# Kernel optimization log

Measured on AMD Instinct MI355X. Metric: run time of the kernel, lower is better.

Reference implementation:

```python
import jax, jax.numpy as jnp
import numpy as np

N_NODES = 100000
N_EDGES = 200000
N_GRAPHS = 4096
NODE_DIM = 256
OUT_DIM = 768
LAYERS = 4
NODE_FEATS = 9
EDGE_FEATS = 3
NODE_VOCAB = 119  # max categorical size across node features (padded)
EDGE_VOCAB = 22   # max categorical size across edge features (padded)


def setup_inputs() -> dict:
    key = jax.random.key(0)
    ks = jax.random.split(key, 16)
    x_cat = jax.random.randint(ks[0], (N_NODES, NODE_FEATS), 0, 2)
    edge_attr = jax.random.randint(ks[1], (N_EDGES, EDGE_FEATS), 0, 2)
    edge_index = jax.random.randint(ks[2], (2, N_EDGES), 0, N_NODES)
    batch = jnp.sort(jax.random.randint(ks[3], (N_NODES,), 0, N_GRAPHS))
    s = 0.02
    node_emb = jax.random.normal(ks[4], (NODE_FEATS, NODE_VOCAB, NODE_DIM), jnp.float32) * s
    edge_emb = jax.random.normal(ks[5], (EDGE_FEATS, EDGE_VOCAB, NODE_DIM), jnp.float32) * s
    W1 = jax.random.normal(ks[6], (LAYERS, NODE_DIM, 2 * NODE_DIM), jnp.float32) * s
    b1 = jnp.zeros((LAYERS, 2 * NODE_DIM), jnp.float32)
    W2 = jax.random.normal(ks[7], (LAYERS, 2 * NODE_DIM, NODE_DIM), jnp.float32) * s
    b2 = jnp.zeros((LAYERS, NODE_DIM), jnp.float32)
    pW1 = jax.random.normal(ks[8], (NODE_DIM, NODE_DIM), jnp.float32) * s
    pb1 = jnp.zeros((NODE_DIM,), jnp.float32)
    pW2 = jax.random.normal(ks[9], (NODE_DIM, OUT_DIM), jnp.float32) * s
    pb2 = jnp.zeros((OUT_DIM,), jnp.float32)
    return {
        "x_cat": x_cat, "edge_attr": edge_attr, "edge_index": edge_index, "batch": batch,
        "node_emb": node_emb, "edge_emb": edge_emb,
        "W1": W1, "b1": b1, "W2": W2, "b2": b2,
        "pW1": pW1, "pb1": pb1, "pW2": pW2, "pb2": pb2,
    }


def _encode(tables, idx):
    # tables: [F, V, D], idx: [N, F] -> sum over features of embedding lookups -> [N, D]
    return jnp.sum(jax.vmap(lambda tbl, i: tbl[i], in_axes=(0, 1))(tables, idx), axis=0)


def reference(x_cat, edge_attr, edge_index, batch, node_emb, edge_emb,
              W1, b1, W2, b2, pW1, pb1, pW2, pb2):
    x = _encode(node_emb, x_cat)          # [N, D]
    e = _encode(edge_emb, edge_attr)      # [E, D]
    src, dst = edge_index[0], edge_index[1]
    for l in range(LAYERS):
        # GINEConv: aggr = sum_{j in N(i)} relu(x_j + e_ij); out = mlp((1+eps)*x_i + aggr), eps=0
        msg = jax.nn.relu(x[src] + e)                                  # [E, D]
        agg = jax.ops.segment_sum(msg, dst, num_segments=N_NODES)     # [N, D]
        h = x + agg
        h = jax.nn.relu(h @ W1[l] + b1[l]) @ W2[l] + b2[l]
        x = jax.nn.relu(h)
    g = jax.ops.segment_sum(x, batch, num_segments=N_GRAPHS)          # [G, D]
    g = jax.nn.relu(g @ pW1 + pb1) @ pW2 + pb2                         # [G, OUT]
    norm = jnp.maximum(jnp.linalg.norm(g, axis=-1, keepdims=True), 1e-12)
    return g / norm
```

## Files before the change

kernel.cpp:

```cpp
#include <hip/hip_runtime.h>

#define N_NODES 100000
#define N_NODES_PAD 100032
#define N_EDGES 200000
#define N_GRAPHS 4096
#define D 256
#define D2 512
#define OUTD 768
#define LAYERS 4
#define NODE_FEATS 9
#define EDGE_FEATS 3
#define NODE_VOCAB 119
#define EDGE_VOCAB 22
#define BM 64
#define GB 8

typedef __attribute__((ext_vector_type(8))) short bf16x8;
typedef __attribute__((ext_vector_type(4))) float f32x4;
typedef unsigned short ushort_t;
typedef unsigned int uint_t;

__device__ __forceinline__ ushort_t f2b(float f) {
    union { float f; uint_t u; } x; x.f = f;
    uint_t r = (x.u + 0x7FFFu + ((x.u >> 16) & 1u)) >> 16;
    return (ushort_t)r;
}
__device__ __forceinline__ float b2f(ushort_t u) {
    union { uint_t u; float f; } x; x.u = ((uint_t)u) << 16;
    return x.f;
}

__device__ __forceinline__ int lower_bound_i(const int* a, int n, int v) {
    int lo = 0, hi = n;
    while (lo < hi) { int mid = (lo + hi) >> 1; if (a[mid] < v) lo = mid + 1; else hi = mid; }
    return lo;
}

__global__ __launch_bounds__(256) void encode_nodes_k(const int* __restrict__ xcat,
                                                      const float* __restrict__ tab,
                                                      ushort_t* __restrict__ X) {
    int n = blockIdx.x, d = threadIdx.x;
    float acc = 0.f;
#pragma unroll
    for (int f = 0; f < NODE_FEATS; ++f) {
        int idx = xcat[n * NODE_FEATS + f];
        acc += tab[((size_t)f * NODE_VOCAB + idx) * D + d];
    }
    X[(size_t)n * D + d] = f2b(acc);
}

__global__ __launch_bounds__(256) void count_k(const int* __restrict__ eidx, int* deg) {
    int e = blockIdx.x * 256 + threadIdx.x;
    if (e < N_EDGES) atomicAdd(&deg[eidx[N_EDGES + e]], 1);
}

#define SCAN_B 1024
__global__ __launch_bounds__(256) void scan1_k(const int* __restrict__ deg,
                                               int* __restrict__ excl, int* __restrict__ bsum) {
    __shared__ int sh[256];
    int b = blockIdx.x, t = threadIdx.x;
    int base = b * SCAN_B + t * 4;
    int d0 = (base + 0) < N_NODES ? deg[base + 0] : 0;
    int d1 = (base + 1) < N_NODES ? deg[base + 1] : 0;
    int d2 = (base + 2) < N_NODES ? deg[base + 2] : 0;
    int d3 = (base + 3) < N_NODES ? deg[base + 3] : 0;
    int s = d0 + d1 + d2 + d3;
    sh[t] = s; __syncthreads();
    for (int off = 1; off < 256; off <<= 1) {
        int x = (t >= off) ? sh[t - off] : 0;
        __syncthreads();
        sh[t] += x;
        __syncthreads();
    }
    int incl = sh[t];
    int ex = incl - s;
    if (base + 0 < N_NODES) excl[base + 0] = ex;
    if (base + 1 < N_NODES) excl[base + 1] = ex + d0;
    if (base + 2 < N_NODES) excl[base + 2] = ex + d0 + d1;
    if (base + 3 < N_NODES) excl[base + 3] = ex + d0 + d1 + d2;
    if (t == 255) bsum[b] = incl;
}

__global__ void scan2_k(int* bsum, int nb) {
    __shared__ int sh[128];
    int t = threadIdx.x;
    int v = (t < nb) ? bsum[t] : 0;
    sh[t] = v; __syncthreads();
    for (int off = 1; off < 128; off <<= 1) {
        int x = (t >= off) ? sh[t - off] : 0;
        __syncthreads();
        sh[t] += x;
        __syncthreads();
    }
    if (t < nb) bsum[t] = sh[t] - v;
}

__global__ __launch_bounds__(256) void scan3_k(int* __restrict__ offs, int* __restrict__ cursor,
                                               const int* __restrict__ bsum) {
    int i = blockIdx.x * 256 + threadIdx.x;
    if (i < N_NODES) {
        int v = offs[i] + bsum[i >> 10];
        offs[i] = v;
        cursor[i] = v;
    }
}

__global__ __launch_bounds__(256) void fill_k(const int* __restrict__ eidx,
                                              const int* __restrict__ eattr,
                                              int* cursor, int2* __restrict__ elist) {
    int e = blockIdx.x * 256 + threadIdx.x;
    if (e < N_EDGES) {
        int src = eidx[e];
        int dst = eidx[N_EDGES + e];
        int pa = eattr[e * EDGE_FEATS + 0] | (eattr[e * EDGE_FEATS + 1] << 8)
               | (eattr[e * EDGE_FEATS + 2] << 16);
        int pos = atomicAdd(&cursor[dst], 1);
        elist[pos] = make_int2(src, pa);
    }
}

__global__ __launch_bounds__(256) void gather_k(const ushort4* __restrict__ X4,
                                                const float4* __restrict__ eemb4,
                                                const int* __restrict__ offs,
                                                const int* __restrict__ deg,
                                                const int2* __restrict__ elist,
                                                ushort4* __restrict__ H4) {
    int n = blockIdx.x * 4 + (threadIdx.x >> 6);
    int lane = threadIdx.x & 63;
    int start = offs[n], dg = deg[n];
    ushort4 xv = X4[(size_t)n * 64 + lane];
    float acc[4] = {b2f(xv.x), b2f(xv.y), b2f(xv.z), b2f(xv.w)};
    for (int i = 0; i < dg; i += 2) {
        bool has1 = (i + 1 < dg);
        int2 s0 = elist[start + i];
        int2 s1 = has1 ? elist[start + i + 1] : s0;
        ushort4 v0 = X4[(size_t)s0.x * 64 + lane];
        ushort4 v1 = X4[(size_t)s1.x * 64 + lane];
        float4 a0 = eemb4[(size_t)((s0.y      ) & 255) * 64 + lane];
        float4 a1 = eemb4[((size_t)EDGE_VOCAB + ((s0.y >> 8) & 255)) * 64 + lane];
        float4 a2 = eemb4[((size_t)2 * EDGE_VOCAB + ((s0.y >> 16) & 255)) * 64 + lane];
        acc[0] += fmaxf(b2f(v0.x) + a0.x + a1.x + a2.x, 0.f);
        acc[1] += fmaxf(b2f(v0.y) + a0.y + a1.y + a2.y, 0.f);
        acc[2] += fmaxf(b2f(v0.z) + a0.z + a1.z + a2.z, 0.f);
        acc[3] += fmaxf(b2f(v0.w) + a0.w + a1.w + a2.w, 0.f);
        if (has1) {
            float4 c0 = eemb4[(size_t)((s1.y      ) & 255) * 64 + lane];
            float4 c1 = eemb4[((size_t)EDGE_VOCAB + ((s1.y >> 8) & 255)) * 64 + lane];
            float4 c2 = eemb4[((size_t)2 * EDGE_VOCAB + ((s1.y >> 16) & 255)) * 64 + lane];
            acc[0] += fmaxf(b2f(v1.x) + c0.x + c1.x + c2.x, 0.f);
            acc[1] += fmaxf(b2f(v1.y) + c0.y + c1.y + c2.y, 0.f);
            acc[2] += fmaxf(b2f(v1.z) + c0.z + c1.z + c2.z, 0.f);
            acc[3] += fmaxf(b2f(v1.w) + c0.w + c1.w + c2.w, 0.f);
        }
    }
    ushort4 hv;
    hv.x = f2b(acc[0]); hv.y = f2b(acc[1]); hv.z = f2b(acc[2]); hv.w = f2b(acc[3]);
    H4[(size_t)n * 64 + lane] = hv;
}

__global__ __launch_bounds__(256) void pack1_k(const float* __restrict__ W1, ushort_t* __restrict__ apack) {
    size_t i = (size_t)blockIdx.x * 256 + threadIdx.x;
    int l = (int)(i >> 14);
    int rem = (int)(i & 16383);
    int ntg = rem >> 9;
    int rem2 = rem & 511;
    int kk = rem2 >> 6;
    int lane = rem2 & 63;
    int n = ntg * 16 + (lane & 15);
    int k0 = kk * 32 + (lane >> 4) * 8;
    const float* w = W1 + ((size_t)l * D + k0) * D2 + n;
    ushort_t* o = apack + i * 8;
#pragma unroll
    for (int j = 0; j < 8; ++j) o[j] = f2b(w[(size_t)j * D2]);
}

__global__ __launch_bounds__(256) void pack2_k(const float* __restrict__ W2, ushort_t* __restrict__ bpack) {
    size_t i = (size_t)blockIdx.x * 256 + threadIdx.x;
    int l = (int)(i >> 14);
    int rem = (int)(i & 16383);
    int ntg = rem >> 10;
    int rem2 = rem & 1023;
    int kk = rem2 >> 6;
    int lane = rem2 & 63;
    int n = ntg * 16 + (lane & 15);
    int k0 = kk * 32 + (lane >> 4) * 8;
    const float* w = W2 + ((size_t)l * D2 + k0) * D + n;
    ushort_t* o = bpack + i * 8;
#pragma unroll
    for (int j = 0; j < 8; ++j) o[j] = f2b(w[(size_t)j * D]);
}

__global__ __launch_bounds__(512, 4) void mlp_k(const ushort_t* __restrict__ H,
                                                const ushort_t* __restrict__ apack,
                                                const float* __restrict__ b1,
                                                const ushort_t* __restrict__ bpack,
                                                const float* __restrict__ b2,
                                                ushort_t* __restrict__ X) {
    __shared__ __align__(16) char hA[BM * 512];
    __shared__ __align__(16) char midh[BM * 512];
    const int t = threadIdx.x;
    const int wid = t >> 6, lane = t & 63;
    const int l15 = lane & 15, g = lane >> 4;
    const size_t r0 = (size_t)blockIdx.x * BM;

    {
        const char* src = (const char*)(H + r0 * D);
#pragma unroll
        for (int c = 0; c < 4; ++c) {
            int Lb = (c * 512 + t) * 16;
            int row = Lb >> 9;
            int Sb = Lb ^ ((row & 7) << 4);
            *(uint4*)(hA + Sb) = *(const uint4*)(src + Lb);
        }
    }

    f32x4 acc2[2][4];
#pragma unroll
    for (int a = 0; a < 2; ++a)
#pragma unroll
        for (int b = 0; b < 4; ++b) { f32x4 z = {0.f,0.f,0.f,0.f}; acc2[a][b] = z; }

    bf16x8 AfA[2], AfB[2], WfA[2], WfB[2];
#pragma unroll
    for (int nt = 0; nt < 2; ++nt)
        AfA[nt] = *(const bf16x8*)(apack + ((size_t)((0 * 16 + wid * 2 + nt) * 8 + 0) * 64 + lane) * 8);

    __syncthreads();

#pragma unroll
    for (int half = 0; half < 2; ++half) {
        f32x4 acc1[2][4];
#pragma unroll
        for (int a = 0; a < 2; ++a)
#pragma unroll
            for (int b = 0; b < 4; ++b) { f32x4 z = {0.f,0.f,0.f,0.f}; acc1[a][b] = z; }

#pragma unroll
        for (int kk = 0; kk < 8; ++kk) {
            bf16x8 Bf[4];
#pragma unroll
            for (int mt = 0; mt < 4; ++mt) {
                int m = mt * 16 + l15;
                Bf[mt] = *(const bf16x8*)(hA + ((m * 512 + (kk * 32 + g * 8) * 2) ^ ((m & 7) << 4)));
            }
            bf16x8* cur = (kk & 1) ? AfB : AfA;
            bf16x8* nxt = (kk & 1) ? AfA : AfB;
            if (kk < 7) {
#pragma unroll
                for (int nt = 0; nt < 2; ++nt)
                    nxt[nt] = *(const bf16x8*)(apack +
                        ((size_t)((half * 16 + wid * 2 + nt) * 8 + kk + 1) * 64 + lane) * 8);
            }
            __builtin_amdgcn_s_setprio(1);
#pragma unroll
            for (int nt = 0; nt < 2; ++nt)
#pragma unroll
                for (int mt = 0; mt < 4; ++mt)
                    acc1[nt][mt] = __builtin_amdgcn_mfma_f32_16x16x32_bf16(cur[nt], Bf[mt], acc1[nt][mt], 0, 0, 0);
            __builtin_amdgcn_s_setprio(0);
        }

#pragma unroll
        for (int nt = 0; nt < 2; ++nt)
            WfA[nt] = *(const bf16x8*)(bpack +
                ((size_t)((wid * 2 + nt) * 16 + half * 8 + 0) * 64 + lane) * 8);

#pragma unroll
        for (int nt = 0; nt < 2; ++nt) {
            int n0l = (wid * 2 + nt) * 16 + g * 4;
            f32x4 bv = *(const f32x4*)(b1 + half * 256 + n0l);
#pragma unroll
            for (int mt = 0; mt < 4; ++mt) {
                int m = mt * 16 + l15;
                ushort_t us[4];
#pragma unroll
                for (int r = 0; r < 4; ++r)
                    us[r] = f2b(fmaxf(acc1[nt][mt][r] + bv[r], 0.f));
                uint2 pk;
                pk.x = (uint_t)us[0] | ((uint_t)us[1] << 16);
                pk.y = (uint_t)us[2] | ((uint_t)us[3] << 16);
                *(uint2*)(midh + ((m * 512 + n0l * 2) ^ ((m & 7) << 4))) = pk;
            }
        }
        __syncthreads();

#pragma unroll
        for (int kk = 0; kk < 8; ++kk) {
            bf16x8 Mf[4];
#pragma unroll
            for (int mt = 0; mt < 4; ++mt) {
                int m = mt * 16 + l15;
                Mf[mt] = *(const bf16x8*)(midh + ((m * 512 + (kk * 32 + g * 8) * 2) ^ ((m & 7) << 4)));
            }
            bf16x8* cur = (kk & 1) ? WfB : WfA;
            bf16x8* nxt = (kk & 1) ? WfA : WfB;
            if (kk < 7) {
#pragma unroll
                for (int nt = 0; nt < 2; ++nt)
                    nxt[nt] = *(const bf16x8*)(bpack +
                        ((size_t)((wid * 2 + nt) * 16 + half * 8 + kk + 1) * 64 + lane) * 8);
            }
            __builtin_amdgcn_s_setprio(1);
#pragma unroll
            for (int nt = 0; nt < 2; ++nt)
#pragma unroll
                for (int mt = 0; mt < 4; ++mt)
                    acc2[nt][mt] = __builtin_amdgcn_mfma_f32_16x16x32_bf16(cur[nt], Mf[mt], acc2[nt][mt], 0, 0, 0);
            __builtin_amdgcn_s_setprio(0);
        }

        if (half == 0) {
#pragma unroll
            for (int nt = 0; nt < 2; ++nt)
                AfA[nt] = *(const bf16x8*)(apack +
                    ((size_t)((1 * 16 + wid * 2 + nt) * 8 + 0) * 64 + lane) * 8);
        }
        __syncthreads();
    }

#pragma unroll
    for (int nt = 0; nt < 2; ++nt) {
        int n0 = (wid * 2 + nt) * 16 + g * 4;
        f32x4 bv = *(const f32x4*)(b2 + n0);
#pragma unroll
        for (int mt = 0; mt < 4; ++mt) {
            int m = mt * 16 + l15;
            ushort_t us[4];
#pragma unroll
            for (int r = 0; r < 4; ++r)
                us[r] = f2b(fmaxf(acc2[nt][mt][r] + bv[r], 0.f));
            uint2 pk;
            pk.x = (uint_t)us[0] | ((uint_t)us[1] << 16);
            pk.y = (uint_t)us[2] | ((uint_t)us[3] << 16);
            *(uint2*)(midh + ((m * 512 + n0 * 2) ^ ((m & 7) << 4))) = pk;
        }
    }
    __syncthreads();
    {
        char* dst = (char*)X + r0 * 512;
#pragma unroll
        for (int j = 0; j < 4; ++j) {
            int Lb = t * 64 + j * 16;
            int row = Lb >> 9;
            int Sb = Lb ^ ((row & 7) << 4);
            *(uint4*)(dst + Lb) = *(const uint4*)(midh + Sb);
        }
    }
}

__global__ __launch_bounds__(256) void final_k(const ushort4* __restrict__ X4,
                                               const int* __restrict__ batch,
                                               const float* __restrict__ pW1,
                                               const float* __restrict__ pb1,
                                               const float* __restrict__ pW2,
                                               const float* __restrict__ pb2,
                                               float* __restrict__ out) {
    __shared__ float gin[GB][D];
    __shared__ float mid[GB][D];
    __shared__ float red[GB][256];
    __shared__ int bnd[GB + 1];
    const int g0 = blockIdx.x * GB, t = threadIdx.x;
    const int wid = t >> 6, lane = t & 63;
    if (t <= GB) bnd[t] = lower_bound_i(batch, N_NODES, g0 + t);
    __syncthreads();

#pragma unroll
    for (int qq = 0; qq < 2; ++qq) {
        int q = wid + qq * 4;
        f32x4 a = {0.f, 0.f, 0.f, 0.f};
        for (int n = bnd[q]; n < bnd[q + 1]; ++n) {
            ushort4 v = X4[(size_t)n * 64 + lane];
            a.x += b2f(v.x); a.y += b2f(v.y); a.z += b2f(v.z); a.w += b2f(v.w);
        }
        *(f32x4*)&gin[q][lane * 4] = a;
    }
    __syncthreads();

    {
        float m_[GB];
        float bb = pb1[t];
#pragma unroll
        for (int q = 0; q < GB; ++q) m_[q] = bb;
        for (int k = 0; k < D; ++k) {
            float w = pW1[(size_t)k * D + t];
#pragma unroll
            for (int q = 0; q < GB; ++q) m_[q] += gin[q][k] * w;
        }
#pragma unroll
        for (int q = 0; q < GB; ++q) mid[q][t] = fmaxf(m_[q], 0.f);
    }
    __syncthreads();

    float a0[GB], a1[GB], a2[GB];
    {
        float b0 = pb2[t], b1_ = pb2[t + 256], b2_ = pb2[t + 512];
#pragma unroll
        for (int q = 0; q < GB; ++q) { a0[q] = b0; a1[q] = b1_; a2[q] = b2_; }
        for (int k = 0; k < D; ++k) {
            float w0 = pW2[(size_t)k * OUTD + t];
            float w1 = pW2[(size_t)k * OUTD + 256 + t];
            float w2 = pW2[(size_t)k * OUTD + 512 + t];
#pragma unroll
            for (int q = 0; q < GB; ++q) {
                float mv = mid[q][k];
                a0[q] += mv * w0; a1[q] += mv * w1; a2[q] += mv * w2;
            }
        }
    }
#pragma unroll
    for (int q = 0; q < GB; ++q)
        red[q][t] = a0[q] * a0[q] + a1[q] * a1[q] + a2[q] * a2[q];
    __syncthreads();
    for (int s = 128; s > 0; s >>= 1) {
        if (t < s) {
#pragma unroll
            for (int q = 0; q < GB; ++q) red[q][t] += red[q][t + s];
        }
        __syncthreads();
    }
#pragma unroll
    for (int q = 0; q < GB; ++q) {
        float inv = 1.f / fmaxf(sqrtf(red[q][0]), 1e-12f);
        out[(size_t)(g0 + q) * OUTD + t]       = a0[q] * inv;
        out[(size_t)(g0 + q) * OUTD + 256 + t] = a1[q] * inv;
        out[(size_t)(g0 + q) * OUTD + 512 + t] = a2[q] * inv;
    }
}

extern "C" void kernel_launch(void* const* d_in, const int* in_sizes, int n_in,
                              void* d_out, int out_size, void* d_ws, size_t ws_size,
                              hipStream_t stream) {
    const int*   x_cat      = (const int*)d_in[0];
    const int*   edge_attr  = (const int*)d_in[1];
    const int*   edge_index = (const int*)d_in[2];
    const int*   batch      = (const int*)d_in[3];
    const float* node_emb   = (const float*)d_in[4];
    const float* edge_emb   = (const float*)d_in[5];
    const float* W1  = (const float*)d_in[6];
    const float* b1  = (const float*)d_in[7];
    const float* W2  = (const float*)d_in[8];
    const float* b2  = (const float*)d_in[9];
    const float* pW1 = (const float*)d_in[10];
    const float* pb1 = (const float*)d_in[11];
    const float* pW2 = (const float*)d_in[12];
    const float* pb2 = (const float*)d_in[13];
    float* out = (float*)d_out;

    char* p = (char*)d_ws;
    auto carve = [&](size_t bytes) { char* q = p; p += (bytes + 255) & ~(size_t)255; return q; };
    ushort_t* X      = (ushort_t*)carve((size_t)N_NODES_PAD * D * 2);
    ushort_t* H      = (ushort_t*)carve((size_t)N_NODES_PAD * D * 2);
    int*      deg    = (int*)carve((size_t)N_NODES * 4);
    int*      offs   = (int*)carve((size_t)(N_NODES + 8) * 4);
    int*      cursor = (int*)carve((size_t)(N_NODES + 8) * 4);
    int*      bsum   = (int*)carve(1024);
    int2*     elist  = (int2*)carve((size_t)N_EDGES * 8);
    ushort_t* apack1 = (ushort_t*)carve((size_t)LAYERS * 32 * 8 * 64 * 8 * 2);
    ushort_t* bpack2 = (ushort_t*)carve((size_t)LAYERS * 16 * 16 * 64 * 8 * 2);

    const int NB = (N_NODES + SCAN_B - 1) / SCAN_B;

    pack1_k<<<256, 256, 0, stream>>>(W1, apack1);
    pack2_k<<<256, 256, 0, stream>>>(W2, bpack2);
    hipMemsetAsync(deg, 0, (size_t)N_NODES * 4, stream);
    count_k<<<(N_EDGES + 255) / 256, 256, 0, stream>>>(edge_index, deg);
    scan1_k<<<NB, 256, 0, stream>>>(deg, offs, bsum);
    scan2_k<<<1, 128, 0, stream>>>(bsum, NB);
    scan3_k<<<(N_NODES + 255) / 256, 256, 0, stream>>>(offs, cursor, bsum);
    fill_k<<<(N_EDGES + 255) / 256, 256, 0, stream>>>(edge_index, edge_attr, cursor, elist);

    encode_nodes_k<<<N_NODES, 256, 0, stream>>>(x_cat, node_emb, X);

    for (int l = 0; l < LAYERS; ++l) {
        gather_k<<<N_NODES / 4, 256, 0, stream>>>((const ushort4*)X, (const float4*)edge_emb,
                                                  offs, deg, elist, (ushort4*)H);
        mlp_k<<<N_NODES_PAD / BM, 512, 0, stream>>>(
            H,
            apack1 + (size_t)l * 32 * 8 * 64 * 8,
            b1 + (size_t)l * D2,
            bpack2 + (size_t)l * 16 * 16 * 64 * 8,
            b2 + (size_t)l * D,
            X);
    }

    final_k<<<N_GRAPHS / GB, 256, 0, stream>>>((const ushort4*)X, batch, pW1, pb1, pW2, pb2, out);
}
```

Measured before the change: 742.3 us.

## Split fused MLP kernel into two GEMM kernels via global intermediate buffer

The fused two-GEMM MLP kernel is split into g1_k (first GEMM + bias + ReLU) and g2_k (second GEMM + bias + ReLU). The 512-wide hidden activation is written to a new global buffer in an MFMA-fragment-friendly layout instead of living in shared memory. This frees LDS and removes block-wide barriers, which may raise occupancy. The cost is an extra round trip of about 100MB through global memory per layer plus an extra launch.

```diff
diff --git a/kernel.cpp b/kernel.cpp
--- a/kernel.cpp
+++ b/kernel.cpp
@@ -190,14 +190,11 @@
     for (int j = 0; j < 8; ++j) o[j] = f2b(w[(size_t)j * D]);
 }
 
-__global__ __launch_bounds__(512, 4) void mlp_k(const ushort_t* __restrict__ H,
-                                                const ushort_t* __restrict__ apack,
-                                                const float* __restrict__ b1,
-                                                const ushort_t* __restrict__ bpack,
-                                                const float* __restrict__ b2,
-                                                ushort_t* __restrict__ X) {
+__global__ __launch_bounds__(512, 4) void g1_k(const ushort_t* __restrict__ H,
+                                               const ushort_t* __restrict__ apack,
+                                               const float* __restrict__ b1,
+                                               ushort_t* __restrict__ midp) {
     __shared__ __align__(16) char hA[BM * 512];
-    __shared__ __align__(16) char midh[BM * 512];
     const int t = threadIdx.x;
     const int wid = t >> 6, lane = t & 63;
     const int l15 = lane & 15, g = lane >> 4;
@@ -214,18 +211,14 @@
         }
     }
 
-    f32x4 acc2[2][4];
-#pragma unroll
-    for (int a = 0; a < 2; ++a)
-#pragma unroll
-        for (int b = 0; b < 4; ++b) { f32x4 z = {0.f,0.f,0.f,0.f}; acc2[a][b] = z; }
-
-    bf16x8 AfA[2], AfB[2], WfA[2], WfB[2];
+    bf16x8 AfA[2], AfB[2];
 #pragma unroll
     for (int nt = 0; nt < 2; ++nt)
         AfA[nt] = *(const bf16x8*)(apack + ((size_t)((0 * 16 + wid * 2 + nt) * 8 + 0) * 64 + lane) * 8);
 
     __syncthreads();
+
+    ushort_t* mblk = midp + r0 * D2;
 
 #pragma unroll
     for (int half = 0; half < 2; ++half) {
@@ -260,10 +253,12 @@
             __builtin_amdgcn_s_setprio(0);
         }
 
-#pragma unroll
-        for (int nt = 0; nt < 2; ++nt)
-            WfA[nt] = *(const bf16x8*)(bpack +
-                ((size_t)((wid * 2 + nt) * 16 + half * 8 + 0) * 64 + lane) * 8);
+        if (half == 0) {
+#pragma unroll
+            for (int nt = 0; nt < 2; ++nt)
+                AfA[nt] = *(const bf16x8*)(apack +
+                    ((size_t)((1 * 16 + wid * 2 + nt) * 8 + 0) * 64 + lane) * 8);
+        }
 
 #pragma unroll
         for (int nt = 0; nt < 2; ++nt) {
@@ -271,7 +266,6 @@
             f32x4 bv = *(const f32x4*)(b1 + half * 256 + n0l);
 #pragma unroll
             for (int mt = 0; mt < 4; ++mt) {
-                int m = mt * 16 + l15;
                 ushort_t us[4];
 #pragma unroll
                 for (int r = 0; r < 4; ++r)
@@ -279,43 +273,56 @@
                 uint2 pk;
                 pk.x = (uint_t)us[0] | ((uint_t)us[1] << 16);
                 pk.y = (uint_t)us[2] | ((uint_t)us[3] << 16);
-                *(uint2*)(midh + ((m * 512 + n0l * 2) ^ ((m & 7) << 4))) = pk;
+                size_t off = (size_t)(mt * 64 + half * 32 + (wid * 2 + nt) * 2 + (g >> 1)) * 128
+                           + l15 * 8 + (g & 1) * 4;
+                *(uint2*)(mblk + off) = pk;
             }
         }
-        __syncthreads();
-
-#pragma unroll
-        for (int kk = 0; kk < 8; ++kk) {
-            bf16x8 Mf[4];
-#pragma unroll
-            for (int mt = 0; mt < 4; ++mt) {
-                int m = mt * 16 + l15;
-                Mf[mt] = *(const bf16x8*)(midh + ((m * 512 + (kk * 32 + g * 8) * 2) ^ ((m & 7) << 4)));
-            }
-            bf16x8* cur = (kk & 1) ? WfB : WfA;
-            bf16x8* nxt = (kk & 1) ? WfA : WfB;
-            if (kk < 7) {
-#pragma unroll
-                for (int nt = 0; nt < 2; ++nt)
-                    nxt[nt] = *(const bf16x8*)(bpack +
-                        ((size_t)((wid * 2 + nt) * 16 + half * 8 + kk + 1) * 64 + lane) * 8);
-            }
-            __builtin_amdgcn_s_setprio(1);
+    }
+}
+
+__global__ __launch_bounds__(512, 4) void g2_k(const ushort_t* __restrict__ midp,
+                                               const ushort_t* __restrict__ bpack,
+                                               const float* __restrict__ b2,
+                                               ushort_t* __restrict__ X) {
+    const int t = threadIdx.x;
+    const int wid = t >> 6, lane = t & 63;
+    const int l15 = lane & 15, g = lane >> 4;
+    const size_t r0 = (size_t)blockIdx.x * BM;
+    const ushort_t* mblk = midp + r0 * D2;
+
+    f32x4 acc2[2][4];
+#pragma unroll
+    for (int a = 0; a < 2; ++a)
+#pragma unroll
+        for (int b = 0; b < 4; ++b) { f32x4 z = {0.f,0.f,0.f,0.f}; acc2[a][b] = z; }
+
+    bf16x8 WfA[2], WfB[2];
+#pragma unroll
+    for (int nt = 0; nt < 2; ++nt)
+        WfA[nt] = *(const bf16x8*)(bpack + ((size_t)((wid * 2 + nt) * 16 + 0) * 64 + lane) * 8);
+
+#pragma unroll
+    for (int kk = 0; kk < 16; ++kk) {
+        bf16x8 Mf[4];
+#pragma unroll
+        for (int mt = 0; mt < 4; ++mt)
+            Mf[mt] = *(const bf16x8*)(mblk + (size_t)(mt * 64 + kk * 4 + g) * 128 + l15 * 8);
+        bf16x8* cur = (kk & 1) ? WfB : WfA;
+        bf16x8* nxt = (kk & 1) ? WfA : WfB;
+        if (kk < 15) {
 #pragma unroll
             for (int nt = 0; nt < 2; ++nt)
-#pragma unroll
-                for (int mt = 0; mt < 4; ++mt)
-                    acc2[nt][mt] = __builtin_amdgcn_mfma_f32_16x16x32_bf16(cur[nt], Mf[mt], acc2[nt][mt], 0, 0, 0);
-            __builtin_amdgcn_s_setprio(0);
-        }
-
-        if (half == 0) {
-#pragma unroll
-            for (int nt = 0; nt < 2; ++nt)
-                AfA[nt] = *(const bf16x8*)(apack +
-                    ((size_t)((1 * 16 + wid * 2 + nt) * 8 + 0) * 64 + lane) * 8);
-        }
-        __syncthreads();
+                nxt[nt] = *(const bf16x8*)(bpack +
+                    ((size_t)((wid * 2 + nt) * 16 + kk + 1) * 64 + lane) * 8);
+        }
+        __builtin_amdgcn_s_setprio(1);
+#pragma unroll
+        for (int nt = 0; nt < 2; ++nt)
+#pragma unroll
+            for (int mt = 0; mt < 4; ++mt)
+                acc2[nt][mt] = __builtin_amdgcn_mfma_f32_16x16x32_bf16(cur[nt], Mf[mt], acc2[nt][mt], 0, 0, 0);
+        __builtin_amdgcn_s_setprio(0);
     }
 
 #pragma unroll
@@ -332,18 +339,7 @@
             uint2 pk;
             pk.x = (uint_t)us[0] | ((uint_t)us[1] << 16);
             pk.y = (uint_t)us[2] | ((uint_t)us[3] << 16);
-            *(uint2*)(midh + ((m * 512 + n0 * 2) ^ ((m & 7) << 4))) = pk;
-        }
-    }
-    __syncthreads();
-    {
-        char* dst = (char*)X + r0 * 512;
-#pragma unroll
-        for (int j = 0; j < 4; ++j) {
-            int Lb = t * 64 + j * 16;
-            int row = Lb >> 9;
-            int Sb = Lb ^ ((row & 7) << 4);
-            *(uint4*)(dst + Lb) = *(const uint4*)(midh + Sb);
+            *(uint2*)(X + (r0 + m) * D + n0) = pk;
         }
     }
 }
@@ -450,6 +446,7 @@
     auto carve = [&](size_t bytes) { char* q = p; p += (bytes + 255) & ~(size_t)255; return q; };
     ushort_t* X      = (ushort_t*)carve((size_t)N_NODES_PAD * D * 2);
     ushort_t* H      = (ushort_t*)carve((size_t)N_NODES_PAD * D * 2);
+    ushort_t* midp   = (ushort_t*)carve((size_t)N_NODES_PAD * D2 * 2);
     int*      deg    = (int*)carve((size_t)N_NODES * 4);
     int*      offs   = (int*)carve((size_t)(N_NODES + 8) * 4);
     int*      cursor = (int*)carve((size_t)(N_NODES + 8) * 4);
@@ -474,13 +471,10 @@
     for (int l = 0; l < LAYERS; ++l) {
         gather_k<<<N_NODES / 4, 256, 0, stream>>>((const ushort4*)X, (const float4*)edge_emb,
                                                   offs, deg, elist, (ushort4*)H);
-        mlp_k<<<N_NODES_PAD / BM, 512, 0, stream>>>(
-            H,
-            apack1 + (size_t)l * 32 * 8 * 64 * 8,
-            b1 + (size_t)l * D2,
-            bpack2 + (size_t)l * 16 * 16 * 64 * 8,
-            b2 + (size_t)l * D,
-            X);
+        g1_k<<<N_NODES_PAD / BM, 512, 0, stream>>>(
+            H, apack1 + (size_t)l * 32 * 8 * 64 * 8, b1 + (size_t)l * D2, midp);
+        g2_k<<<N_NODES_PAD / BM, 512, 0, stream>>>(
+            midp, bpack2 + (size_t)l * 16 * 16 * 64 * 8, b2 + (size_t)l * D, X);
     }
 
     final_k<<<N_GRAPHS / GB, 256, 0, stream>>>((const ushort4*)X, batch, pW1, pb1, pW2, pb2, out);
```

New measurement: 768.6 us. +3.5%, slower.
